# Performance work log

Measured on AMD Instinct MI355X. Metric: run time of the kernel, lower is better.

The kernel has to match this reference:

```python
import jax, jax.numpy as jnp
import numpy as np

B, T, C, H, E, TOPK, DR = 2, 2048, 768, 3072, 8, 2, 24


def setup_inputs() -> dict:
    key = jax.random.key(0)
    ks = jax.random.split(key, 16)
    std = 0.02
    n = lambda k, shape, s=std: (s * jax.random.normal(k, shape)).astype(jnp.float32)
    emb = jax.random.normal(ks[3], (E, DR), dtype=jnp.float32)
    emb = emb / (jnp.linalg.norm(emb, axis=-1, keepdims=True) + 1e-8)
    return {
        "x": jax.random.normal(ks[0], (B, T, C), dtype=jnp.float32),
        "router_w": n(ks[1], (E, C)),
        "probe_w": n(ks[2], (DR, C)),
        "router_emb": emb,
        "fatigue": jnp.zeros((E,), jnp.float32),
        "energy": jnp.ones((E,), jnp.float32),
        "w_fast1": n(ks[4], (E, C, H)),
        "w_slow1": n(ks[5], (E, C, H)),
        "h_fast1": n(ks[6], (E, C, H), 0.005),
        "m_gate1": jax.random.uniform(ks[7], (E,), dtype=jnp.float32),
        "b1": jnp.zeros((E, H), jnp.float32),
        "w_fast2": n(ks[8], (E, H, C)),
        "w_slow2": n(ks[9], (E, H, C)),
        "h_fast2": n(ks[10], (E, H, C), 0.005),
        "m_gate2": jax.random.uniform(ks[11], (E,), dtype=jnp.float32),
        "b2": jnp.zeros((E, C), jnp.float32),
    }


def _normalize(v, axis=-1, eps=1e-12):
    # matches F.normalize: v / max(||v||, eps)
    return v / jnp.maximum(jnp.linalg.norm(v, axis=axis, keepdims=True), eps)


def reference(x, router_w, probe_w, router_emb, fatigue, energy,
              w_fast1, w_slow1, h_fast1, m_gate1, b1,
              w_fast2, w_slow2, h_fast2, m_gate2, b2):
    Bd, Td, Cd = x.shape
    # --- router logits with biology-inspired biases ---
    logits = jnp.einsum('btc,ec->bte', x, router_w)            # nn.Linear, no bias
    tok_proxy = x.mean(axis=-1, keepdims=True)                  # [B,T,1]
    router_gain = jnp.linalg.norm(router_emb, axis=-1)          # [E]
    base_bias = 0.02 * tok_proxy                                # broadcasts over E
    gain_bias = 0.02 * tok_proxy * router_gain                  # [B,T,E]
    tok_unit = _normalize(jnp.einsum('btc,dc->btd', x, probe_w))
    align_bias = 0.02 * jnp.einsum('btd,ed->bte', tok_unit, _normalize(router_emb))
    logits = logits + base_bias + gain_bias + align_bias + 0.1 * energy - 0.1 * fatigue
    # --- top-k gating ---
    g, idx = jax.lax.top_k(logits, TOPK)                        # [B,T,K]
    gates = jax.nn.softmax(g, axis=-1)
    N = Bd * Td
    gates_full = jnp.zeros((N, E), x.dtype).at[
        jnp.arange(N)[:, None], idx.reshape(N, TOPK)].set(gates.reshape(N, TOPK))
    flat_x = x.reshape(N, Cd)
    # --- expert dispatch: dynamic W = w_fast + m_gate*w_slow + H_fast ---
    def body(acc, p):
        wf1, ws1, hf1, mg1, bb1, wf2, ws2, hf2, mg2, bb2, ge = p
        W1 = wf1 + mg1 * ws1 + hf1                              # [C,H]
        h = jnp.square(jnp.maximum(flat_x @ W1 + bb1, 0.0))     # relu(y)^2
        W2 = wf2 + mg2 * ws2 + hf2                              # [H,C]
        y = h @ W2 + bb2
        return acc + ge[:, None] * y, None
    out, _ = jax.lax.scan(
        body, jnp.zeros((N, Cd), x.dtype),
        (w_fast1, w_slow1, h_fast1, m_gate1, b1,
         w_fast2, w_slow2, h_fast2, m_gate2, b2, gates_full.T))
    return out.reshape(Bd, Td, Cd)
```

## Files before the change

### kernel.cpp

```cpp
#include <hip/hip_runtime.h>

typedef unsigned short u16;
typedef __attribute__((ext_vector_type(8))) short short8;
typedef __attribute__((ext_vector_type(8))) unsigned short ushort8;
typedef __attribute__((ext_vector_type(4))) unsigned short ushort4v;
typedef __attribute__((ext_vector_type(4))) float f32x4;

static constexpr int Cdim = 768;
static constexpr int Hdim = 3072;
static constexpr int Edim = 8;
static constexpr int Ntok = 4096;
static constexpr int DRc  = 24;
static constexpr int NSLOT = Ntok * 2;
static constexpr int NCHUNK = 8;
static constexpr int CCH = Cdim / NCHUNK;
static constexpr int KS2 = 3;
static constexpr int KC2 = Hdim / KS2;
static constexpr int MAXROWS = 71;
static constexpr int NPREP = 4608;

static constexpr size_t OFF_XB   = 0;
static constexpr size_t OFF_W1T  = 6291456;
static constexpr size_t OFF_W2T  = 44040192;
static constexpr size_t OFF_HBUF = 81788928;
static constexpr size_t OFF_XT   = OFF_HBUF;
static constexpr size_t OFF_PART = OFF_HBUF + 12582912;
static constexpr size_t OFF_YB   = OFF_W1T;
static constexpr size_t OFF_TOK  = 132120576;
static constexpr size_t OFF_RM   = 132251648;
static constexpr size_t OFF_NR   = 132252160;
static constexpr size_t OFF_CNT  = 132382720;
static constexpr size_t OFF_OFFS = 132382752;
static constexpr size_t OFF_TSLOT= 132382784;
static constexpr size_t OFF_TG   = 132448320;

__device__ __forceinline__ u16 f2bf(float f) {
  unsigned u = __builtin_bit_cast(unsigned, f);
  u += 0x7fffu + ((u >> 16) & 1u);
  return (u16)(u >> 16);
}

__device__ __forceinline__ float bf2f(u16 v) {
  unsigned u = ((unsigned)v) << 16;
  return __builtin_bit_cast(float, u);
}

__device__ __forceinline__ void gld16(const u16* g, u16* l) {
  __builtin_amdgcn_global_load_lds((const __attribute__((address_space(1))) unsigned int*)g,
                                   (__attribute__((address_space(3))) unsigned int*)l,
                                   16, 0, 0);
}

__device__ __forceinline__ int xcd_remap(int p, int nwg) {
  int q = nwg >> 3, rem = nwg & 7;
  int x = p & 7, i = p >> 3;
  return (x < rem ? x * (q + 1) : rem * (q + 1) + (x - rem) * q) + i;
}

__global__ __launch_bounds__(256)
void prep_x2_kernel(const float* __restrict__ x, u16* __restrict__ x16,
                    float* __restrict__ xT) {
  __shared__ float tile[64][65];
  const int c0 = blockIdx.x * 64;
  const int t0 = blockIdx.y * 64;
  const int tid = threadIdx.x;
  const int row = tid >> 4, col = (tid & 15) * 4;
  #pragma unroll
  for (int i = 0; i < 4; i++) {
    int r = row + i * 16;
    size_t idx = (size_t)(t0 + r) * Cdim + c0 + col;
    float4 v = *(const float4*)(x + idx);
    tile[r][col + 0] = v.x; tile[r][col + 1] = v.y;
    tile[r][col + 2] = v.z; tile[r][col + 3] = v.w;
    ushort4v o = { f2bf(v.x), f2bf(v.y), f2bf(v.z), f2bf(v.w) };
    *reinterpret_cast<ushort4v*>(x16 + idx) = o;
  }
  __syncthreads();
  const int c = tid >> 2, tg = (tid & 3) * 16;
  #pragma unroll
  for (int q = 0; q < 4; q++) {
    float4 w;
    w.x = tile[tg + q * 4 + 0][c];
    w.y = tile[tg + q * 4 + 1][c];
    w.z = tile[tg + q * 4 + 2][c];
    w.w = tile[tg + q * 4 + 3][c];
    *reinterpret_cast<float4*>(xT + (size_t)(c0 + c) * Ntok + t0 + tg + q * 4) = w;
  }
}

template<int R, int CCOL>
__device__ __forceinline__ void prep_wt_body(const float* __restrict__ wf,
                                             const float* __restrict__ wsl,
                                             const float* __restrict__ hf, float m,
                                             u16* __restrict__ outw, int e, int r0, int c0,
                                             unsigned* lds) {
  const size_t base = (size_t)e * R * CCOL;
  const int t = threadIdx.x;
  {
    const int rp = t >> 5;
    const int col4 = (t & 31) * 4;
    const int c2w = (t & 31) * 2;
    #pragma unroll
    for (int i = 0; i < 8; i++) {
      int r = i * 8 + rp;
      size_t idx = base + (size_t)(r0 + r) * CCOL + c0 + col4;
      float4 a = *(const float4*)(wf + idx);
      float4 b = *(const float4*)(wsl + idx);
      float4 h = *(const float4*)(hf + idx);
      unsigned u0 = (unsigned)f2bf(fmaf(m, b.x, a.x) + h.x)
                  | ((unsigned)f2bf(fmaf(m, b.y, a.y) + h.y) << 16);
      unsigned u1 = (unsigned)f2bf(fmaf(m, b.z, a.z) + h.z)
                  | ((unsigned)f2bf(fmaf(m, b.w, a.w) + h.w) << 16);
      lds[c2w * 65 + r] = u0;
      lds[(c2w + 1) * 65 + r] = u1;
    }
  }
  __syncthreads();
  {
    const int c2 = t >> 2;
    const int rseg = (t & 3) * 16;
    const unsigned* cp = lds + c2 * 65 + rseg;
    unsigned in4[16];
    #pragma unroll
    for (int j = 0; j < 4; j++)
      *reinterpret_cast<uint4*>(&in4[j * 4]) = *reinterpret_cast<const uint4*>(cp + j * 4);
    unsigned lo[8], hi[8];
    #pragma unroll
    for (int j = 0; j < 8; j++) {
      unsigned a = in4[2 * j], b = in4[2 * j + 1];
      lo[j] = (a & 0xffffu) | (b << 16);
      hi[j] = (a >> 16) | (b & 0xffff0000u);
    }
    size_t ob = ((size_t)e * CCOL + c0 + 2 * c2) * R + r0 + rseg;
    *reinterpret_cast<uint4*>(outw + ob)          = *reinterpret_cast<const uint4*>(&lo[0]);
    *reinterpret_cast<uint4*>(outw + ob + 8)      = *reinterpret_cast<const uint4*>(&lo[4]);
    *reinterpret_cast<uint4*>(outw + ob + R)      = *reinterpret_cast<const uint4*>(&hi[0]);
    *reinterpret_cast<uint4*>(outw + ob + R + 8)  = *reinterpret_cast<const uint4*>(&hi[4]);
  }
}

__global__ __launch_bounds__(256)
void prep_wt2_kernel(const float* __restrict__ wf1, const float* __restrict__ ws1,
                     const float* __restrict__ hf1, const float* __restrict__ mg1,
                     u16* __restrict__ o1,
                     const float* __restrict__ wf2, const float* __restrict__ ws2,
                     const float* __restrict__ hf2, const float* __restrict__ mg2,
                     u16* __restrict__ o2) {
  __shared__ unsigned lds[64 * 65];
  int bid = blockIdx.x;
  if (bid < 2304) {
    int e = bid / 288, rem = bid % 288;
    int xx = rem % 12, yy = rem / 12;
    prep_wt_body<768, 3072>(wf1, ws1, hf1, mg1[e], o1, e, xx * 64, yy * 128, lds);
  } else {
    bid -= 2304;
    int e = bid / 288, rem = bid % 288;
    int xx = rem % 48, yy = rem / 48;
    prep_wt_body<3072, 768>(wf2, ws2, hf2, mg2[e], o2, e, xx * 64, yy * 128, lds);
  }
}

__global__ __launch_bounds__(256)
void logits_part_kernel(const float* __restrict__ xT, const float* __restrict__ router_w,
                        const float* __restrict__ probe_w, float* __restrict__ part) {
  const int t = blockIdx.x * 256 + threadIdx.x;
  const int cB = blockIdx.y * CCH;
  float racc[Edim] = {};
  float pacc[DRc] = {};
  float sacc = 0.f;
  for (int ci = 0; ci < CCH; ci++) {
    int c = cB + ci;
    float xv = xT[(size_t)c * Ntok + t];
    sacc += xv;
    #pragma unroll
    for (int ee = 0; ee < Edim; ee++) racc[ee] = fmaf(xv, router_w[ee * Cdim + c], racc[ee]);
    #pragma unroll
    for (int d = 0; d < DRc; d++) pacc[d] = fmaf(xv, probe_w[d * Cdim + c], pacc[d]);
  }
  float* pb = part + (size_t)blockIdx.y * 33 * Ntok + t;
  #pragma unroll
  for (int ee = 0; ee < Edim; ee++) pb[(size_t)ee * Ntok] = racc[ee];
  #pragma unroll
  for (int d = 0; d < DRc; d++) pb[(size_t)(8 + d) * Ntok] = pacc[d];
  pb[(size_t)32 * Ntok] = sacc;
}

__global__ __launch_bounds__(256)
void router_fin_kernel(const float* __restrict__ part, const float* __restrict__ emb,
                       const float* __restrict__ fatigue, const float* __restrict__ energy,
                       int* __restrict__ counts, int* __restrict__ tok_list,
                       int4* __restrict__ tokslot, float2* __restrict__ tokgate) {
  const int t = blockIdx.x * 256 + threadIdx.x;
  float v[33];
  #pragma unroll
  for (int o = 0; o < 33; o++) {
    float s = 0.f;
    #pragma unroll
    for (int ch = 0; ch < NCHUNK; ch++)
      s += part[((size_t)ch * 33 + o) * Ntok + t];
    v[o] = s;
  }
  const float* racc = v;
  const float* pacc = v + 8;
  float proxy = v[32] / 768.f;
  float pn2 = 0.f;
  #pragma unroll
  for (int d = 0; d < DRc; d++) pn2 += pacc[d] * pacc[d];
  float pnorm = sqrtf(pn2);
  float logitv[Edim];
  #pragma unroll
  for (int ee = 0; ee < Edim; ee++) {
    float g2 = 0.f, dote = 0.f;
    #pragma unroll
    for (int d = 0; d < DRc; d++) {
      float ev = emb[ee * DRc + d];
      g2 += ev * ev;
      dote += pacc[d] * ev;
    }
    float gain = sqrtf(g2);
    float align = dote / (fmaxf(pnorm, 1e-12f) * fmaxf(gain, 1e-12f));
    logitv[ee] = racc[ee] + 0.02f * proxy * (1.f + gain) + 0.02f * align
               + 0.1f * energy[ee] - 0.1f * fatigue[ee];
  }
  int e0 = 0; float b0v = logitv[0];
  #pragma unroll
  for (int ee = 1; ee < Edim; ee++) if (logitv[ee] > b0v) { b0v = logitv[ee]; e0 = ee; }
  int e1 = -1; float b1v = -3.4e38f;
  #pragma unroll
  for (int ee = 0; ee < Edim; ee++) if (ee != e0 && logitv[ee] > b1v) { b1v = logitv[ee]; e1 = ee; }
  float texp = expf(b1v - b0v);
  float g0 = 1.f / (1.f + texp);
  float g1 = texp / (1.f + texp);
  int p0 = atomicAdd(&counts[e0], 1);
  tok_list[e0 * Ntok + p0] = t;
  int p1 = atomicAdd(&counts[e1], 1);
  tok_list[e1 * Ntok + p1] = t;
  tokslot[t] = make_int4(e0, p0, e1, p1);
  tokgate[t] = make_float2(g0, g1);
}

__global__ void offsets_kernel(const int* __restrict__ counts, int* __restrict__ offs,
                               int* __restrict__ rowmap, int* __restrict__ nrows) {
  if (threadIdx.x == 0) {
    int r = 0, nr = 0;
    for (int e = 0; e < Edim; e++) {
      offs[e] = r;
      int ne = counts[e];
      for (int tb = 0; tb < ne; tb += 128) rowmap[nr++] = (e << 16) | (tb >> 7);
      r += ne;
    }
    nrows[0] = nr;
  }
}

__global__ __launch_bounds__(256)
void fc1_kernel(const u16* __restrict__ x16, const u16* __restrict__ W1T,
                const float* __restrict__ b1, const int* __restrict__ counts,
                const int* __restrict__ offs, const int* __restrict__ tok_list,
                const int* __restrict__ rowmap, const int* __restrict__ nrows,
                u16* __restrict__ h_buf) {
  const int l = xcd_remap(blockIdx.x, MAXROWS * 24);
  const int r = l / 24;
  if (r >= nrows[0]) return;
  const int hB = l % 24;
  const int rm = rowmap[r];
  const int e = rm >> 16;
  const int tokBase = (rm & 0xffff) << 7;
  const int n_e = counts[e];
  const int hBase = hB * 128;
  __shared__ u16 As[4096];
  __shared__ u16 Bs[4096];
  __shared__ int toks[128];
  const int tid = threadIdx.x;
  if (tid < 128) {
    int s = tokBase + tid;
    toks[tid] = (s < n_e) ? tok_list[e * Ntok + s] : 0;
  }
  __syncthreads();
  const int lane = tid & 63, wv = tid >> 6;
  const int wr = wv >> 1, wc = wv & 1;
  const int sRow = lane >> 2, sSlot = lane & 3;
  const int kbOff = (sSlot ^ ((sRow >> 1) & 3)) * 8;
  const int rA0 = wv * 16 + sRow, rA1 = 64 + rA0;
  const u16* pA0 = x16 + (size_t)toks[rA0] * Cdim + kbOff;
  const u16* pA1 = x16 + (size_t)toks[rA1] * Cdim + kbOff;
  const u16* pB0 = W1T + ((size_t)e * Hdim + hBase + rA0) * Cdim + kbOff;
  const u16* pB1 = W1T + ((size_t)e * Hdim + hBase + rA1) * Cdim + kbOff;
  const int stOff = wv * 512 + lane * 8;
  const int fr = lane & 15;
  const int qsw = (((lane >> 4) ^ ((fr >> 1) & 3))) * 8;
  f32x4 acc[4][4] = {};
  for (int it = 0; it < 24; it++) {
    int k0 = it * 32;
    gld16(pA0 + k0, &As[stOff]);
    gld16(pA1 + k0, &As[2048 + stOff]);
    gld16(pB0 + k0, &Bs[stOff]);
    gld16(pB1 + k0, &Bs[2048 + stOff]);
    __syncthreads();
    short8 aF[4], bF[4];
    #pragma unroll
    for (int m = 0; m < 4; m++)
      aF[m] = *reinterpret_cast<const short8*>(&As[(wr * 64 + m * 16 + fr) * 32 + qsw]);
    #pragma unroll
    for (int n = 0; n < 4; n++)
      bF[n] = *reinterpret_cast<const short8*>(&Bs[(wc * 64 + n * 16 + fr) * 32 + qsw]);
    #pragma unroll
    for (int m = 0; m < 4; m++)
      #pragma unroll
      for (int n = 0; n < 4; n++)
        acc[m][n] = __builtin_amdgcn_mfma_f32_16x16x32_bf16(aF[m], bF[n], acc[m][n], 0, 0, 0);
    __syncthreads();
  }
  const int rq = (lane >> 4) * 4;
  float bias[4];
  #pragma unroll
  for (int n = 0; n < 4; n++) bias[n] = b1[(size_t)e * Hdim + hBase + wc * 64 + n * 16 + fr];
  const int rowB = offs[e] + tokBase;
  #pragma unroll
  for (int m = 0; m < 4; m++) {
    #pragma unroll
    for (int j = 0; j < 4; j++) {
      int rl = wr * 64 + m * 16 + rq + j;
      if (tokBase + rl < n_e) {
        size_t rb = (size_t)(rowB + rl) * Hdim + hBase + wc * 64 + fr;
        #pragma unroll
        for (int n = 0; n < 4; n++) {
          float v = fmaxf(acc[m][n][j] + bias[n], 0.f);
          h_buf[rb + n * 16] = f2bf(v * v);
        }
      }
    }
  }
}

__global__ __launch_bounds__(256)
void fc2_kernel(const u16* __restrict__ h_buf, const u16* __restrict__ W2T,
                const float* __restrict__ b2, const int* __restrict__ counts,
                const int* __restrict__ offs, const int* __restrict__ rowmap,
                const int* __restrict__ nrows, u16* __restrict__ ybuf) {
  const int l = xcd_remap(blockIdx.x, MAXROWS * 18);
  const int r = l / 18;
  if (r >= nrows[0]) return;
  const int xb = l % 18;
  const int rm = rowmap[r];
  const int e = rm >> 16;
  const int tokBase = (rm & 0xffff) << 7;
  const int n_e = counts[e];
  const int kch = xb / 6;
  const int cBase = (xb % 6) * 128;
  const size_t kOff = (size_t)kch * KC2;
  __shared__ u16 As[4096];
  __shared__ u16 Bs[4096];
  const int tid = threadIdx.x;
  const int lane = tid & 63, wv = tid >> 6;
  const int wr = wv >> 1, wc = wv & 1;
  const int sRow = lane >> 2, sSlot = lane & 3;
  const int kbOff = (sSlot ^ ((sRow >> 1) & 3)) * 8;
  const int rA0 = wv * 16 + sRow, rA1 = 64 + rA0;
  const int slotB = offs[e] + tokBase;
  const int s0 = min(slotB + rA0, NSLOT - 1);
  const int s1 = min(slotB + rA1, NSLOT - 1);
  const u16* pA0 = h_buf + (size_t)s0 * Hdim + kOff + kbOff;
  const u16* pA1 = h_buf + (size_t)s1 * Hdim + kOff + kbOff;
  const u16* pB0 = W2T + ((size_t)e * Cdim + cBase + rA0) * Hdim + kOff + kbOff;
  const u16* pB1 = W2T + ((size_t)e * Cdim + cBase + rA1) * Hdim + kOff + kbOff;
  const int stOff = wv * 512 + lane * 8;
  const int fr = lane & 15;
  const int qsw = (((lane >> 4) ^ ((fr >> 1) & 3))) * 8;
  f32x4 acc[4][4] = {};
  for (int it = 0; it < KC2 / 32; it++) {
    int k0 = it * 32;
    gld16(pA0 + k0, &As[stOff]);
    gld16(pA1 + k0, &As[2048 + stOff]);
    gld16(pB0 + k0, &Bs[stOff]);
    gld16(pB1 + k0, &Bs[2048 + stOff]);
    __syncthreads();
    short8 aF[4], bF[4];
    #pragma unroll
    for (int m = 0; m < 4; m++)
      aF[m] = *reinterpret_cast<const short8*>(&As[(wr * 64 + m * 16 + fr) * 32 + qsw]);
    #pragma unroll
    for (int n = 0; n < 4; n++)
      bF[n] = *reinterpret_cast<const short8*>(&Bs[(wc * 64 + n * 16 + fr) * 32 + qsw]);
    #pragma unroll
    for (int m = 0; m < 4; m++)
      #pragma unroll
      for (int n = 0; n < 4; n++)
        acc[m][n] = __builtin_amdgcn_mfma_f32_16x16x32_bf16(aF[m], bF[n], acc[m][n], 0, 0, 0);
    __syncthreads();
  }
  const int rq = (lane >> 4) * 4;
  float bias[4];
  #pragma unroll
  for (int n = 0; n < 4; n++)
    bias[n] = (kch == 0) ? b2[(size_t)e * Cdim + cBase + wc * 64 + n * 16 + fr] : 0.f;
  u16* yb = ybuf + (size_t)kch * NSLOT * Cdim;
  #pragma unroll
  for (int m = 0; m < 4; m++) {
    #pragma unroll
    for (int j = 0; j < 4; j++) {
      int rl = wr * 64 + m * 16 + rq + j;
      if (tokBase + rl < n_e) {
        u16* ob = yb + (size_t)(slotB + rl) * Cdim + cBase + wc * 64 + fr;
        #pragma unroll
        for (int n = 0; n < 4; n++)
          ob[n * 16] = f2bf(acc[m][n][j] + bias[n]);
      }
    }
  }
}

__global__ __launch_bounds__(256)
void gather_kernel(const u16* __restrict__ ybuf, const int4* __restrict__ tokslot,
                   const float2* __restrict__ tokgate, const int* __restrict__ offs,
                   float* __restrict__ out) {
  const int gid = blockIdx.x * 256 + threadIdx.x;
  const int t = gid / 192;
  const int c4 = (gid - t * 192) * 4;
  int4 ts = tokslot[t];
  float2 g = tokgate[t];
  size_t s0 = (size_t)(offs[ts.x] + ts.y) * Cdim + c4;
  size_t s1 = (size_t)(offs[ts.z] + ts.w) * Cdim + c4;
  const size_t K1 = (size_t)NSLOT * Cdim;
  float acc0[4] = {}, acc1[4] = {};
  #pragma unroll
  for (int k = 0; k < KS2; k++) {
    ushort4v a = *reinterpret_cast<const ushort4v*>(ybuf + k * K1 + s0);
    ushort4v b = *reinterpret_cast<const ushort4v*>(ybuf + k * K1 + s1);
    #pragma unroll
    for (int j = 0; j < 4; j++) { acc0[j] += bf2f(a[j]); acc1[j] += bf2f(b[j]); }
  }
  float4 o;
  o.x = g.x * acc0[0] + g.y * acc1[0];
  o.y = g.x * acc0[1] + g.y * acc1[1];
  o.z = g.x * acc0[2] + g.y * acc1[2];
  o.w = g.x * acc0[3] + g.y * acc1[3];
  *reinterpret_cast<float4*>(out + (size_t)t * Cdim + c4) = o;
}

extern "C" void kernel_launch(void* const* d_in, const int* in_sizes, int n_in,
                              void* d_out, int out_size, void* d_ws, size_t ws_size,
                              hipStream_t stream) {
  const float* x        = (const float*)d_in[0];
  const float* router_w = (const float*)d_in[1];
  const float* probe_w  = (const float*)d_in[2];
  const float* emb      = (const float*)d_in[3];
  const float* fatigue  = (const float*)d_in[4];
  const float* energy   = (const float*)d_in[5];
  const float* wf1      = (const float*)d_in[6];
  const float* ws1      = (const float*)d_in[7];
  const float* hf1      = (const float*)d_in[8];
  const float* mg1      = (const float*)d_in[9];
  const float* b1       = (const float*)d_in[10];
  const float* wf2      = (const float*)d_in[11];
  const float* ws2      = (const float*)d_in[12];
  const float* hf2      = (const float*)d_in[13];
  const float* mg2      = (const float*)d_in[14];
  const float* b2       = (const float*)d_in[15];
  float* out = (float*)d_out;
  char* ws = (char*)d_ws;

  u16*    x16       = (u16*)(ws + OFF_XB);
  u16*    W1T       = (u16*)(ws + OFF_W1T);
  u16*    W2T       = (u16*)(ws + OFF_W2T);
  u16*    hbuf      = (u16*)(ws + OFF_HBUF);
  float*  xT        = (float*)(ws + OFF_XT);
  float*  part      = (float*)(ws + OFF_PART);
  u16*    ybuf      = (u16*)(ws + OFF_YB);
  int*    tok_list  = (int*)(ws + OFF_TOK);
  int*    rowmap    = (int*)(ws + OFF_RM);
  int*    nrows     = (int*)(ws + OFF_NR);
  int*    counts    = (int*)(ws + OFF_CNT);
  int*    offs      = (int*)(ws + OFF_OFFS);
  int4*   tokslot   = (int4*)(ws + OFF_TSLOT);
  float2* tokgate   = (float2*)(ws + OFF_TG);

  hipMemsetAsync(counts, 0, 64, stream);

  prep_x2_kernel<<<dim3(Cdim / 64, Ntok / 64), 256, 0, stream>>>(x, x16, xT);
  logits_part_kernel<<<dim3(Ntok / 256, NCHUNK), 256, 0, stream>>>(xT, router_w, probe_w, part);
  router_fin_kernel<<<Ntok / 256, 256, 0, stream>>>(part, emb, fatigue, energy,
                                                    counts, tok_list, tokslot, tokgate);
  prep_wt2_kernel<<<NPREP, 256, 0, stream>>>(wf1, ws1, hf1, mg1, W1T,
                                             wf2, ws2, hf2, mg2, W2T);
  offsets_kernel<<<1, 64, 0, stream>>>(counts, offs, rowmap, nrows);
  fc1_kernel<<<MAXROWS * 24, 256, 0, stream>>>(x16, W1T, b1, counts, offs, tok_list,
                                               rowmap, nrows, hbuf);
  fc2_kernel<<<MAXROWS * 18, 256, 0, stream>>>(hbuf, W2T, b2, counts, offs,
                                               rowmap, nrows, ybuf);
  gather_kernel<<<Ntok * 192 / 256, 256, 0, stream>>>(ybuf, tokslot, tokgate, offs, out);
  (void)in_sizes; (void)n_in; (void)out_size; (void)ws_size;
}
```

Before: 345.9 us.

## Fuse weight prep into neighbouring kernels to overlap with x prep and fc1

Splits the combined weight-prep kernel: fc1 weight prep is merged into the x conversion/transpose kernel, and fc2 weight prep is appended as extra blocks of the fc1 GEMM kernel. This removes separate launches and lets the bandwidth-heavy W2 prep run alongside the fc1 matrix compute and fill slots left by idle fc1 blocks. Shared memory is unified into one buffer per kernel. It risks contention between the memory-bound prep blocks and the GEMM blocks.

```diff
diff --git a/kernel.cpp b/kernel.cpp
--- a/kernel.cpp
+++ b/kernel.cpp
@@ -17,7 +17,7 @@
 static constexpr int KS2 = 3;
 static constexpr int KC2 = Hdim / KS2;
 static constexpr int MAXROWS = 71;
-static constexpr int NPREP = 4608;
+static constexpr int NFC1 = MAXROWS * 24;
 
 static constexpr size_t OFF_XB   = 0;
 static constexpr size_t OFF_W1T  = 6291456;
@@ -57,37 +57,6 @@
   return (x < rem ? x * (q + 1) : rem * (q + 1) + (x - rem) * q) + i;
 }
 
-__global__ __launch_bounds__(256)
-void prep_x2_kernel(const float* __restrict__ x, u16* __restrict__ x16,
-                    float* __restrict__ xT) {
-  __shared__ float tile[64][65];
-  const int c0 = blockIdx.x * 64;
-  const int t0 = blockIdx.y * 64;
-  const int tid = threadIdx.x;
-  const int row = tid >> 4, col = (tid & 15) * 4;
-  #pragma unroll
-  for (int i = 0; i < 4; i++) {
-    int r = row + i * 16;
-    size_t idx = (size_t)(t0 + r) * Cdim + c0 + col;
-    float4 v = *(const float4*)(x + idx);
-    tile[r][col + 0] = v.x; tile[r][col + 1] = v.y;
-    tile[r][col + 2] = v.z; tile[r][col + 3] = v.w;
-    ushort4v o = { f2bf(v.x), f2bf(v.y), f2bf(v.z), f2bf(v.w) };
-    *reinterpret_cast<ushort4v*>(x16 + idx) = o;
-  }
-  __syncthreads();
-  const int c = tid >> 2, tg = (tid & 3) * 16;
-  #pragma unroll
-  for (int q = 0; q < 4; q++) {
-    float4 w;
-    w.x = tile[tg + q * 4 + 0][c];
-    w.y = tile[tg + q * 4 + 1][c];
-    w.z = tile[tg + q * 4 + 2][c];
-    w.w = tile[tg + q * 4 + 3][c];
-    *reinterpret_cast<float4*>(xT + (size_t)(c0 + c) * Ntok + t0 + tg + q * 4) = w;
-  }
-}
-
 template<int R, int CCOL>
 __device__ __forceinline__ void prep_wt_body(const float* __restrict__ wf,
                                              const float* __restrict__ wsl,
@@ -140,23 +109,45 @@
 }
 
 __global__ __launch_bounds__(256)
-void prep_wt2_kernel(const float* __restrict__ wf1, const float* __restrict__ ws1,
-                     const float* __restrict__ hf1, const float* __restrict__ mg1,
-                     u16* __restrict__ o1,
-                     const float* __restrict__ wf2, const float* __restrict__ ws2,
-                     const float* __restrict__ hf2, const float* __restrict__ mg2,
-                     u16* __restrict__ o2) {
-  __shared__ unsigned lds[64 * 65];
+void fused_pre1_kernel(const float* __restrict__ x, u16* __restrict__ x16,
+                       float* __restrict__ xT,
+                       const float* __restrict__ wf1, const float* __restrict__ ws1,
+                       const float* __restrict__ hf1, const float* __restrict__ mg1,
+                       u16* __restrict__ W1T) {
+  __shared__ unsigned lsbuf[64 * 65];
   int bid = blockIdx.x;
-  if (bid < 2304) {
+  if (bid < 768) {
+    float* tile = reinterpret_cast<float*>(lsbuf);
+    const int c0 = (bid % 12) * 64;
+    const int t0 = (bid / 12) * 64;
+    const int tid = threadIdx.x;
+    const int row = tid >> 4, col = (tid & 15) * 4;
+    #pragma unroll
+    for (int i = 0; i < 4; i++) {
+      int r = row + i * 16;
+      size_t idx = (size_t)(t0 + r) * Cdim + c0 + col;
+      float4 v = *(const float4*)(x + idx);
+      tile[r * 65 + col + 0] = v.x; tile[r * 65 + col + 1] = v.y;
+      tile[r * 65 + col + 2] = v.z; tile[r * 65 + col + 3] = v.w;
+      ushort4v o = { f2bf(v.x), f2bf(v.y), f2bf(v.z), f2bf(v.w) };
+      *reinterpret_cast<ushort4v*>(x16 + idx) = o;
+    }
+    __syncthreads();
+    const int c = tid >> 2, tg = (tid & 3) * 16;
+    #pragma unroll
+    for (int q = 0; q < 4; q++) {
+      float4 w;
+      w.x = tile[(tg + q * 4 + 0) * 65 + c];
+      w.y = tile[(tg + q * 4 + 1) * 65 + c];
+      w.z = tile[(tg + q * 4 + 2) * 65 + c];
+      w.w = tile[(tg + q * 4 + 3) * 65 + c];
+      *reinterpret_cast<float4*>(xT + (size_t)(c0 + c) * Ntok + t0 + tg + q * 4) = w;
+    }
+  } else {
+    bid -= 768;
     int e = bid / 288, rem = bid % 288;
     int xx = rem % 12, yy = rem / 12;
-    prep_wt_body<768, 3072>(wf1, ws1, hf1, mg1[e], o1, e, xx * 64, yy * 128, lds);
-  } else {
-    bid -= 2304;
-    int e = bid / 288, rem = bid % 288;
-    int xx = rem % 48, yy = rem / 48;
-    prep_wt_body<3072, 768>(wf2, ws2, hf2, mg2[e], o2, e, xx * 64, yy * 128, lds);
+    prep_wt_body<768, 3072>(wf1, ws1, hf1, mg1[e], W1T, e, xx * 64, yy * 128, lsbuf);
   }
 }
 
@@ -254,12 +245,26 @@
 }
 
 __global__ __launch_bounds__(256)
-void fc1_kernel(const u16* __restrict__ x16, const u16* __restrict__ W1T,
-                const float* __restrict__ b1, const int* __restrict__ counts,
-                const int* __restrict__ offs, const int* __restrict__ tok_list,
-                const int* __restrict__ rowmap, const int* __restrict__ nrows,
-                u16* __restrict__ h_buf) {
-  const int l = xcd_remap(blockIdx.x, MAXROWS * 24);
+void fused_fc1p2_kernel(const u16* __restrict__ x16, const u16* __restrict__ W1T,
+                        const float* __restrict__ b1, const int* __restrict__ counts,
+                        const int* __restrict__ offs, const int* __restrict__ tok_list,
+                        const int* __restrict__ rowmap, const int* __restrict__ nrows,
+                        u16* __restrict__ h_buf,
+                        const float* __restrict__ wf2, const float* __restrict__ ws2,
+                        const float* __restrict__ hf2, const float* __restrict__ mg2,
+                        u16* __restrict__ W2T) {
+  __shared__ unsigned smem4[4224];
+  if (blockIdx.x >= NFC1) {
+    int bid = blockIdx.x - NFC1;
+    int e = bid / 288, rem = bid % 288;
+    int xx = rem % 48, yy = rem / 48;
+    prep_wt_body<3072, 768>(wf2, ws2, hf2, mg2[e], W2T, e, xx * 64, yy * 128, smem4);
+    return;
+  }
+  u16* As = reinterpret_cast<u16*>(smem4);
+  u16* Bs = As + 4096;
+  int* toks = reinterpret_cast<int*>(As + 8192);
+  const int l = xcd_remap(blockIdx.x, NFC1);
   const int r = l / 24;
   if (r >= nrows[0]) return;
   const int hB = l % 24;
@@ -268,9 +273,6 @@
   const int tokBase = (rm & 0xffff) << 7;
   const int n_e = counts[e];
   const int hBase = hB * 128;
-  __shared__ u16 As[4096];
-  __shared__ u16 Bs[4096];
-  __shared__ int toks[128];
   const int tid = threadIdx.x;
   if (tid < 128) {
     int s = tokBase + tid;
@@ -292,18 +294,18 @@
   f32x4 acc[4][4] = {};
   for (int it = 0; it < 24; it++) {
     int k0 = it * 32;
-    gld16(pA0 + k0, &As[stOff]);
-    gld16(pA1 + k0, &As[2048 + stOff]);
-    gld16(pB0 + k0, &Bs[stOff]);
-    gld16(pB1 + k0, &Bs[2048 + stOff]);
+    gld16(pA0 + k0, As + stOff);
+    gld16(pA1 + k0, As + 2048 + stOff);
+    gld16(pB0 + k0, Bs + stOff);
+    gld16(pB1 + k0, Bs + 2048 + stOff);
     __syncthreads();
     short8 aF[4], bF[4];
     #pragma unroll
     for (int m = 0; m < 4; m++)
-      aF[m] = *reinterpret_cast<const short8*>(&As[(wr * 64 + m * 16 + fr) * 32 + qsw]);
+      aF[m] = *reinterpret_cast<const short8*>(As + (wr * 64 + m * 16 + fr) * 32 + qsw);
     #pragma unroll
     for (int n = 0; n < 4; n++)
-      bF[n] = *reinterpret_cast<const short8*>(&Bs[(wc * 64 + n * 16 + fr) * 32 + qsw]);
+      bF[n] = *reinterpret_cast<const short8*>(Bs + (wc * 64 + n * 16 + fr) * 32 + qsw);
     #pragma unroll
     for (int m = 0; m < 4; m++)
       #pragma unroll
@@ -477,15 +479,15 @@
 
   hipMemsetAsync(counts, 0, 64, stream);
 
-  prep_x2_kernel<<<dim3(Cdim / 64, Ntok / 64), 256, 0, stream>>>(x, x16, xT);
+  fused_pre1_kernel<<<768 + 2304, 256, 0, stream>>>(x, x16, xT,
+                                                    wf1, ws1, hf1, mg1, W1T);
   logits_part_kernel<<<dim3(Ntok / 256, NCHUNK), 256, 0, stream>>>(xT, router_w, probe_w, part);
   router_fin_kernel<<<Ntok / 256, 256, 0, stream>>>(part, emb, fatigue, energy,
                                                     counts, tok_list, tokslot, tokgate);
-  prep_wt2_kernel<<<NPREP, 256, 0, stream>>>(wf1, ws1, hf1, mg1, W1T,
-                                             wf2, ws2, hf2, mg2, W2T);
   offsets_kernel<<<1, 64, 0, stream>>>(counts, offs, rowmap, nrows);
-  fc1_kernel<<<MAXROWS * 24, 256, 0, stream>>>(x16, W1T, b1, counts, offs, tok_list,
-                                               rowmap, nrows, hbuf);
+  fused_fc1p2_kernel<<<NFC1 + 2304, 256, 0, stream>>>(x16, W1T, b1, counts, offs, tok_list,
+                                                      rowmap, nrows, hbuf,
+                                                      wf2, ws2, hf2, mg2, W2T);
   fc2_kernel<<<MAXROWS * 18, 256, 0, stream>>>(hbuf, W2T, b2, counts, offs,
                                                rowmap, nrows, ybuf);
   gather_kernel<<<Ntok * 192 / 256, 256, 0, stream>>>(ybuf, tokslot, tokgate, offs, out);
```

Result: no change. 341.2 us (-1.3%).
